# Kernel tuning notes

Hardware: AMD Instinct MI355X
Metric: run time of the kernel (lower is better)

The kernel has to match this reference:

```python
import jax, jax.numpy as jnp
import numpy as np

N = 200000          # number of nodes (objects)
H = 64              # hidden_size
ARITIES = [1, 2, 3] # arity per relation
NTUP = [250000, 250000, 250000]  # ground atoms per relation


def setup_inputs() -> dict:
    key = jax.random.key(0)
    ks = jax.random.split(key, 32)
    inp = {"node_states": jax.random.normal(ks[0], (N, H), jnp.float32)}
    i = 1
    for r, (a, t) in enumerate(zip(ARITIES, NTUP)):
        inp[f"rel{r}_idx"] = jax.random.randint(ks[i], (t * a,), 0, N, dtype=jnp.int32).astype(jnp.int64); i += 1
        d = a * H
        s = (2.0 / d) ** 0.5
        inp[f"w1_r{r}"] = jax.random.normal(ks[i], (d, d), jnp.float32) * s; i += 1
        inp[f"b1_r{r}"] = jnp.zeros((d,), jnp.float32)
        inp[f"w2_r{r}"] = jax.random.normal(ks[i], (d, d), jnp.float32) * s; i += 1
        inp[f"b2_r{r}"] = jnp.zeros((d,), jnp.float32)
    su = (1.0 / (2 * H)) ** 0.5
    inp["wu1"] = jax.random.normal(ks[i], (2 * H, 2 * H), jnp.float32) * su; i += 1
    inp["bu1"] = jnp.zeros((2 * H,), jnp.float32)
    inp["wu2"] = jax.random.normal(ks[i], (2 * H, H), jnp.float32) * su
    inp["bu2"] = jnp.zeros((H,), jnp.float32)
    return inp


def reference(node_states, rel0_idx, rel1_idx, rel2_idx,
              w1_r0, b1_r0, w2_r0, b2_r0,
              w1_r1, b1_r1, w2_r1, b2_r1,
              w1_r2, b1_r2, w2_r2, b2_r2,
              wu1, bu1, wu2, bu2):
    sum_msg = jnp.zeros_like(node_states)
    rels = [(ARITIES[0], rel0_idx, w1_r0, b1_r0, w2_r0, b2_r0),
            (ARITIES[1], rel1_idx, w1_r1, b1_r1, w2_r1, b2_r1),
            (ARITIES[2], rel2_idx, w1_r2, b1_r2, w2_r2, b2_r2)]
    for a, idx, w1, b1, w2, b2 in rels:
        # gather node states for each ground atom: [T, a*H]
        x = node_states[idx].reshape(-1, a * H)
        h = jax.nn.relu(x @ w1 + b1)
        msg = (h @ w2 + b2).reshape(-1, H)  # [T*a, H]
        # scatter-add messages back to their nodes
        sum_msg = sum_msg.at[idx].add(msg)
    z = jnp.concatenate([sum_msg, node_states], axis=1)  # [N, 2H]
    return jax.nn.relu(z @ wu1 + bu1) @ wu2 + bu2
```

## Files before the change

kernel.cpp:

```cpp
#include <hip/hip_runtime.h>

#define H 64

typedef __attribute__((ext_vector_type(8))) __bf16 bf16x8;
typedef __attribute__((ext_vector_type(4))) float f32x4;
typedef unsigned short u16;
typedef unsigned int u32;

union F8 { bf16x8 b; u16 u[8]; uint4 q; };

__device__ __forceinline__ u16 f2bf(float f) {
    union { __bf16 h; u16 u; } v; v.h = (__bf16)f; return v.u;
}
__device__ __forceinline__ float bf2f(u16 x) {
    return __uint_as_float((u32)x << 16);
}
__device__ __forceinline__ unsigned swz(int col, int k, int K) {
    return ((unsigned)(col * K + k) * 2u) ^ (((unsigned)col & 7u) << 4);
}

struct Seg { const float* src; unsigned dstBytes; int K; int N; };
struct Segs { Seg s[8]; };

__global__ __launch_bounds__(256) void conv_weights(Segs segs, char* out) {
    Seg sg = segs.s[blockIdx.y];
    int total = sg.K * sg.N;
    char* dst = out + sg.dstBytes;
    for (int e = blockIdx.x * 256 + threadIdx.x; e < total; e += gridDim.x * 256) {
        int k = e / sg.N, n = e % sg.N;
        *(u16*)(dst + swz(n, k, sg.K)) = f2bf(sg.src[e]);
    }
}

struct PrepA { const float4* nsrc; ushort4* ndst; int n4; Segs segs; char* wout; u32* cnt; int N; };

__global__ __launch_bounds__(256) void prep_kernel(PrepA a) {
    if (blockIdx.y == 0) {
        for (int i = blockIdx.x * 256 + threadIdx.x; i < a.n4; i += gridDim.x * 256) {
            float4 f = a.nsrc[i];
            ushort4 o;
            o.x = f2bf(f.x); o.y = f2bf(f.y); o.z = f2bf(f.z); o.w = f2bf(f.w);
            a.ndst[i] = o;
        }
    } else if (blockIdx.y == 1) {
        for (int s = 0; s < 8; ++s) {
            Seg sg = a.segs.s[s];
            int total = sg.K * sg.N;
            char* dst = a.wout + sg.dstBytes;
            for (int e = blockIdx.x * 256 + threadIdx.x; e < total; e += gridDim.x * 256) {
                int k = e / sg.N, n = e % sg.N;
                *(u16*)(dst + swz(n, k, sg.K)) = f2bf(sg.src[e]);
            }
        }
    } else {
        for (int i = blockIdx.x * 256 + threadIdx.x; i < a.N; i += gridDim.x * 256)
            a.cnt[i] = 0u;
    }
}

__global__ __launch_bounds__(512) void scan_blocks(u32* __restrict__ data,
                                                   u32* __restrict__ sums, int n) {
    __shared__ u32 s[512];
    int tid = threadIdx.x, i = blockIdx.x * 512 + tid;
    u32 v = (i < n) ? data[i] : 0u;
    s[tid] = v; __syncthreads();
    for (int d = 1; d < 512; d <<= 1) {
        u32 t = (tid >= d) ? s[tid - d] : 0u; __syncthreads();
        s[tid] += t; __syncthreads();
    }
    if (i < n) data[i] = s[tid] - v;
    if (tid == 511) sums[blockIdx.x] = s[511];
}

__global__ __launch_bounds__(512) void scan_sums(u32* __restrict__ sums, int nb) {
    __shared__ u32 s[512];
    int tid = threadIdx.x;
    u32 v = (tid < nb) ? sums[tid] : 0u;
    s[tid] = v; __syncthreads();
    for (int d = 1; d < 512; d <<= 1) {
        u32 t = (tid >= d) ? s[tid - d] : 0u; __syncthreads();
        s[tid] += t; __syncthreads();
    }
    if (tid < nb) sums[tid] = s[tid] - v;
}

__global__ __launch_bounds__(512) void scan_add(u32* __restrict__ data,
                                                const u32* __restrict__ sums, int n) {
    int i = blockIdx.x * 512 + threadIdx.x;
    if (i < n) data[i] += sums[blockIdx.x];
}

struct OFix {
    const int* idx0; const int* idx1; const int* idx2;
    int m0, m1, m2;
    const u32* base; const u32* pre; u32* ord;
};

__global__ __launch_bounds__(256) void ord_fix(OFix a) {
    const int Mtot = a.m0 + a.m1 + a.m2;
    for (int e = blockIdx.x * 256 + threadIdx.x; e < Mtot; e += gridDim.x * 256) {
        int lm = e, node;
        if (lm < a.m0) node = a.idx0[lm];
        else { lm -= a.m0; if (lm < a.m1) node = a.idx1[lm]; else node = a.idx2[lm - a.m1]; }
        a.ord[a.base[node] + a.pre[e]] = (u32)e;
    }
}

struct Scat {
    const int* idx0; const int* idx1; const int* idx2;
    int m0, m1, m2;
    const u32* base; const u32* pre;
    const u16* msgu; u16* msgs;
};

__global__ __launch_bounds__(256) void scatter_msg(Scat a) {
    const int Mtot = a.m0 + a.m1 + a.m2;
    const int CH = Mtot * 8;
    for (int c = blockIdx.x * 256 + threadIdx.x; c < CH; c += gridDim.x * 256) {
        const int e = c >> 3, q = c & 7;
        int lm = e, node;
        if (lm < a.m0) node = a.idx0[lm];
        else { lm -= a.m0; if (lm < a.m1) node = a.idx1[lm]; else node = a.idx2[lm - a.m1]; }
        const u32 slot = a.base[node] + a.pre[e];
        ((uint4*)(a.msgs + (size_t)slot * 64))[q] =
            ((const uint4*)(a.msgu + (size_t)e * 64))[q];
    }
}

template<int A>
__device__ __forceinline__ void msg_body(
    const u16* __restrict__ nsb, const int* __restrict__ idx,
    const u16* __restrict__ w1T, const float* __restrict__ b1,
    const u16* __restrict__ w2T, const float* __restrict__ b2,
    u16* __restrict__ msgR, int T, int bid, u16* Wl, u16* h1)
{
    constexpr int D    = A * 64;
    constexpr int KS   = D / 32;
    constexpr int NT   = D / 16;
    constexpr bool DUAL = (A == 1);
    constexpr bool CS   = (A > 1);
    constexpr int RF   = CS ? 2 : 1;
    constexpr int WH   = (A == 3) ? 3 : 1;
    constexpr int NTH  = NT / WH;
    constexpr int NTW  = CS ? NTH / 2 : NTH;
    constexpr int COLH = D / WH;
    constexpr int NPF  = (DUAL ? 2 * D * D : COLH * D) / 8 / 512;
    constexpr int NB   = WH * NTW;

    const int tid  = threadIdx.x;
    const int lane = tid & 63;
    const int w    = tid >> 6;
    const int g    = lane >> 4;
    const int lr   = lane & 15;
    const int rg   = CS ? (w >> 1) : w;
    const int cg   = CS ? (w & 1) : 0;

    const int tile = bid * 128;

    auto stage = [&](const u16* gsrc) {
#pragma unroll
        for (int i = 0; i < NPF; ++i) {
            const u16* gp = gsrc + ((i * 512 + tid) << 3);
            u16* lp = Wl + ((i * 512 + (w << 6)) << 3);
            __builtin_amdgcn_global_load_lds(
                (const __attribute__((address_space(1))) void*)gp,
                (__attribute__((address_space(3))) void*)lp, 16, 0, 0);
        }
    };

    bf16x8 a1[RF][KS];
#pragma unroll
    for (int rf = 0; rf < RF; ++rf) {
        const int trow = tile + rg * (16 * RF) + rf * 16 + lr;
        const int tl   = trow < T ? trow : T - 1;
        int nodes[A];
#pragma unroll
        for (int s = 0; s < A; ++s) nodes[s] = idx[(long)tl * A + s];
#pragma unroll
        for (int kk = 0; kk < KS; ++kk) {
            const u16* p = nsb + (long)nodes[kk >> 1] * H + ((kk & 1) * 32 + g * 8);
            F8 t; t.q = *(const uint4*)p;
            a1[rf][kk] = t.b;
        }
    }

    float bias1[NB], bias2[NB];
#pragma unroll
    for (int i = 0; i < NB; ++i) {
        const int jg = (i / NTW) * NTH + cg * NTW + (i % NTW);
        bias1[i] = b1[jg * 16 + lr];
        bias2[i] = b2[jg * 16 + lr];
    }

#pragma unroll
    for (int hh = 0; hh < WH; ++hh) {
        stage(DUAL ? w1T : (w1T + (size_t)hh * COLH * D));
        asm volatile("s_waitcnt vmcnt(0)" ::: "memory");
        __syncthreads();

#pragma unroll
        for (int jl = 0; jl < NTW; ++jl) {
            const int jc = cg * NTW + jl;
            const int jg = hh * NTH + jc;
            f32x4 acc0 = {0.f, 0.f, 0.f, 0.f};
            f32x4 acc1 = {0.f, 0.f, 0.f, 0.f};
#pragma unroll
            for (int kk = 0; kk < KS; ++kk) {
                F8 bf; bf.q = *(const uint4*)((const char*)Wl + swz(jc * 16 + lr, kk * 32 + g * 8, D));
                acc0 = __builtin_amdgcn_mfma_f32_16x16x32_bf16(a1[0][kk], bf.b, acc0, 0, 0, 0);
                if constexpr (CS)
                    acc1 = __builtin_amdgcn_mfma_f32_16x16x32_bf16(a1[1][kk], bf.b, acc1, 0, 0, 0);
            }
#pragma unroll
            for (int r = 0; r < 4; ++r) {
                const int row0 = rg * (16 * RF) + g * 4 + r;
                float v0 = acc0[r] + bias1[hh * NTW + jl]; v0 = v0 > 0.f ? v0 : 0.f;
                *(u16*)((char*)h1 + swz(row0, jg * 16 + lr, D)) = f2bf(v0);
                if constexpr (CS) {
                    float v1 = acc1[r] + bias1[hh * NTW + jl]; v1 = v1 > 0.f ? v1 : 0.f;
                    *(u16*)((char*)h1 + swz(row0 + 16, jg * 16 + lr, D)) = f2bf(v1);
                }
            }
        }
        if constexpr (!DUAL) __syncthreads();
    }

    bf16x8 a2[RF][KS];
#pragma unroll
    for (int rf = 0; rf < RF; ++rf) {
        const int row = rg * (16 * RF) + rf * 16 + lr;
#pragma unroll
        for (int kk = 0; kk < KS; ++kk) {
            F8 t; t.q = *(const uint4*)((const char*)h1 + swz(row, kk * 32 + g * 8, D));
            a2[rf][kk] = t.b;
        }
    }

#pragma unroll
    for (int hh = 0; hh < WH; ++hh) {
        if constexpr (!DUAL) {
            stage(w2T + (size_t)hh * COLH * D);
            asm volatile("s_waitcnt vmcnt(0)" ::: "memory");
            __syncthreads();
        }
        const char* W2base = DUAL ? (const char*)(Wl + D * D) : (const char*)Wl;

#pragma unroll
        for (int jl = 0; jl < NTW; ++jl) {
            const int jc = cg * NTW + jl;
            const int jg = hh * NTH + jc;
            f32x4 acc0 = {0.f, 0.f, 0.f, 0.f};
            f32x4 acc1 = {0.f, 0.f, 0.f, 0.f};
#pragma unroll
            for (int kk = 0; kk < KS; ++kk) {
                F8 bf; bf.q = *(const uint4*)(W2base + swz(jc * 16 + lr, kk * 32 + g * 8, D));
                acc0 = __builtin_amdgcn_mfma_f32_16x16x32_bf16(a2[0][kk], bf.b, acc0, 0, 0, 0);
                if constexpr (CS)
                    acc1 = __builtin_amdgcn_mfma_f32_16x16x32_bf16(a2[1][kk], bf.b, acc1, 0, 0, 0);
            }
            const int gc   = jg * 16 + lr;
            const int slot = gc >> 6;
            const int cs_  = gc & 63;
#pragma unroll
            for (int r = 0; r < 4; ++r) {
                const int a0 = rg * (16 * RF) + g * 4 + r;
                const int m0 = a0 * A + slot;
                unsigned b0 = (((unsigned)(m0 * 64 + cs_)) * 2u) ^ (((unsigned)m0 & 7u) << 4);
                *(u16*)((char*)h1 + b0) = f2bf(acc0[r] + bias2[hh * NTW + jl]);
                if constexpr (CS) {
                    const int m1 = (a0 + 16) * A + slot;
                    unsigned b1x = (((unsigned)(m1 * 64 + cs_)) * 2u) ^ (((unsigned)m1 & 7u) << 4);
                    *(u16*)((char*)h1 + b1x) = f2bf(acc1[r] + bias2[hh * NTW + jl]);
                }
            }
        }
        if constexpr (!DUAL) { if (hh + 1 < WH) __syncthreads(); }
    }

    if constexpr (CS) {
        __syncthreads();
        const int mbase = tile * A;
        constexpr int CH = 128 * A * 16;
#pragma unroll
        for (int i = 0; i < CH / 512; ++i) {
            const int c    = i * 512 + tid;
            const int row  = c >> 4;
            const int atom = row / A;
            if (tile + atom < T) {
                unsigned byte = (((unsigned)(row * 64 + (c & 15) * 4)) * 2u) ^ (((unsigned)row & 7u) << 4);
                uint2 v = *(const uint2*)((const char*)h1 + byte);
                *(uint2*)(msgR + (size_t)(mbase + row) * 64 + (c & 15) * 4) = v;
            }
        }
    } else {
        const bool full  = (tile + 128 <= T);
#pragma unroll
        for (int i = 0; i < 16 * A; i += 4) {
            int ml   = i + (lane >> 4);
            int mrow = w * 16 * A + ml;
            bool ok  = full || ((tile + w * 16 + ml / A) < T);
            if (ok) {
                unsigned byte = (((unsigned)(mrow * 64 + (lane & 15) * 4)) * 2u) ^ (((unsigned)mrow & 7u) << 4);
                uint2 v = *(const uint2*)((const char*)h1 + byte);
                *(uint2*)(msgR + (size_t)((tile * A) + mrow) * 64 + (lane & 15) * 4) = v;
            }
        }
    }
}

struct MegaA {
    const u16* nsb;
    const int* idx0; const int* idx1; const int* idx2;
    int m0, m1, m2, t0, t1, t2;
    u32* cnt; u32* pre;
    const u16 *w10, *w20, *w11, *w21, *w12, *w22;
    const float *b10, *b20, *b11, *b21, *b12, *b22;
    u16* msgu;
    int nrank, nb2, nb1, nb0, striped;
};

__global__ __launch_bounds__(512, 4) void mega_kernel(MegaA a) {
    __shared__ __align__(16) u16 sm[36864];
    const int bx = blockIdx.x;
    int kind, id;
    if (a.striped) {
        const int strip = 4 * a.nrank;
        if (bx < strip) {
            if ((bx & 3) == 3) { kind = 1; id = bx >> 2; }
            else               { kind = 0; id = bx - (bx >> 2); }
        } else { kind = 0; id = bx - a.nrank; }
    } else {
        if (bx < a.nrank) { kind = 1; id = bx; }
        else              { kind = 0; id = bx - a.nrank; }
    }

    if (kind == 1) {
        const int Mtot = a.m0 + a.m1 + a.m2;
        for (int e = id * 512 + (int)threadIdx.x; e < Mtot; e += a.nrank * 512) {
            int lm = e, node;
            if (lm < a.m0) node = a.idx0[lm];
            else { lm -= a.m0; if (lm < a.m1) node = a.idx1[lm]; else node = a.idx2[lm - a.m1]; }
            a.pre[e] = atomicAdd(a.cnt + node, 1u);
        }
        return;
    }

    const int nmsg = a.nb2 + a.nb1 + a.nb0;
    if (id >= nmsg) return;
    if (id < a.nb2)
        msg_body<3>(a.nsb, a.idx2, a.w12, a.b12, a.w22, a.b22,
                    a.msgu + (size_t)(a.m0 + a.m1) * 64, a.t2, id, sm, sm + 12288);
    else if (id < a.nb2 + a.nb1)
        msg_body<2>(a.nsb, a.idx1, a.w11, a.b11, a.w21, a.b21,
                    a.msgu + (size_t)a.m0 * 64, a.t1, id - a.nb2, sm, sm + 16384);
    else
        msg_body<1>(a.nsb, a.idx0, a.w10, a.b10, a.w20, a.b20,
                    a.msgu, a.t0, id - a.nb2 - a.nb1, sm, sm + 8192);
}

template<int A>
__global__ __launch_bounds__(512) void rel_kernel(
    const float* __restrict__ ns, const int* __restrict__ idx,
    const u16* __restrict__ w1T, const float* __restrict__ b1,
    const u16* __restrict__ w2T, const float* __restrict__ b2,
    float* __restrict__ dout, int T)
{
    constexpr int D  = A * 64;
    constexpr int KS = D / 32;
    constexpr int NT = D / 16;
    constexpr bool DUAL = (A == 1);
    __shared__ __align__(16) u16 Wl[(DUAL ? 2 : 1) * D * D];
    __shared__ __align__(16) u16 h1[128 * D];

    const int tid  = threadIdx.x;
    const int lane = tid & 63;
    const int w    = tid >> 6;
    const int g    = lane >> 4;
    const int lr   = lane & 15;

    const int tile = blockIdx.x * 128;
    const int trow = tile + w * 16 + lr;
    const int tl   = trow < T ? trow : T - 1;

    {
        constexpr int NV = (DUAL ? 2 : 1) * D * D / 8;
        const uint4* s4 = (const uint4*)w1T;
        uint4* d4 = (uint4*)Wl;
#pragma unroll
        for (int i = 0; i < NV / 512; ++i) d4[i * 512 + tid] = s4[i * 512 + tid];
    }

    int nodes[A];
#pragma unroll
    for (int s = 0; s < A; ++s) nodes[s] = idx[(long)tl * A + s];

    bf16x8 a1[KS];
#pragma unroll
    for (int kk = 0; kk < KS; ++kk) {
        const float* p = ns + (long)nodes[kk >> 1] * H + ((kk & 1) * 32 + g * 8);
        float4 f0 = *(const float4*)p;
        float4 f1 = *(const float4*)(p + 4);
        F8 t;
        t.u[0] = f2bf(f0.x); t.u[1] = f2bf(f0.y); t.u[2] = f2bf(f0.z); t.u[3] = f2bf(f0.w);
        t.u[4] = f2bf(f1.x); t.u[5] = f2bf(f1.y); t.u[6] = f2bf(f1.z); t.u[7] = f2bf(f1.w);
        a1[kk] = t.b;
    }

    float bias1[NT];
#pragma unroll
    for (int j = 0; j < NT; ++j) bias1[j] = b1[j * 16 + lr];

    __syncthreads();

#pragma unroll
    for (int j = 0; j < NT; ++j) {
        f32x4 acc = {0.f, 0.f, 0.f, 0.f};
#pragma unroll
        for (int kk = 0; kk < KS; ++kk) {
            F8 bf; bf.q = *(const uint4*)((const char*)Wl + swz(j * 16 + lr, kk * 32 + g * 8, D));
            acc = __builtin_amdgcn_mfma_f32_16x16x32_bf16(a1[kk], bf.b, acc, 0, 0, 0);
        }
#pragma unroll
        for (int r = 0; r < 4; ++r) {
            float vv = acc[r] + bias1[j];
            vv = vv > 0.f ? vv : 0.f;
            int row = w * 16 + g * 4 + r;
            *(u16*)((char*)h1 + swz(row, j * 16 + lr, D)) = f2bf(vv);
        }
    }

    const char* W2base;
    if constexpr (!DUAL) {
        __syncthreads();
        const uint4* s4 = (const uint4*)w2T;
        uint4* d4 = (uint4*)Wl;
        constexpr int NV = D * D / 8;
#pragma unroll
        for (int i = 0; i < NV / 512; ++i) d4[i * 512 + tid] = s4[i * 512 + tid];
        W2base = (const char*)Wl;
    } else {
        W2base = (const char*)(Wl + D * D);
    }

    bf16x8 a2[KS];
#pragma unroll
    for (int kk = 0; kk < KS; ++kk) {
        int row = w * 16 + lr;
        F8 t; t.q = *(const uint4*)((const char*)h1 + swz(row, kk * 32 + g * 8, D));
        a2[kk] = t.b;
    }

    float bias2[NT];
#pragma unroll
    for (int j = 0; j < NT; ++j) bias2[j] = b2[j * 16 + lr];

    int  nodes2[A][4];
    bool pred[4];
#pragma unroll
    for (int r = 0; r < 4; ++r) {
        int t  = tile + w * 16 + g * 4 + r;
        int tc = t < T ? t : T - 1;
        pred[r] = t < T;
#pragma unroll
        for (int s = 0; s < A; ++s) nodes2[s][r] = idx[(long)tc * A + s];
    }
    if constexpr (!DUAL) __syncthreads();

#pragma unroll
    for (int j = 0; j < NT; ++j) {
        f32x4 acc = {0.f, 0.f, 0.f, 0.f};
#pragma unroll
        for (int kk = 0; kk < KS; ++kk) {
            F8 bf; bf.q = *(const uint4*)(W2base + swz(j * 16 + lr, kk * 32 + g * 8, D));
            acc = __builtin_amdgcn_mfma_f32_16x16x32_bf16(a2[kk], bf.b, acc, 0, 0, 0);
        }
        const int slot = j >> 2;
        const int coff = (j & 3) * 16 + lr;
#pragma unroll
        for (int r = 0; r < 4; ++r) {
            if (pred[r])
                unsafeAtomicAdd(dout + (long)nodes2[slot][r] * H + coff, acc[r] + bias2[j]);
        }
    }
}

template<int MODE>
__global__ __launch_bounds__(512) void update_kernel(
    const float* __restrict__ ns, const u16* __restrict__ nsb,
    const float* __restrict__ sum,
    const u32* __restrict__ ord, const u32* __restrict__ base,
    const u16* __restrict__ msg, int Mtot,
    const u16* __restrict__ wu1T, const float* __restrict__ bu1,
    const u16* __restrict__ wu2T, const float* __restrict__ bu2,
    float* __restrict__ out, int N)
{
    __shared__ __align__(16) u16 Wl[128 * 128 + 64 * 128];
    __shared__ __align__(16) u16 h[128 * 128];

    const int tid  = threadIdx.x;
    const int lane = tid & 63;
    const int w    = tid >> 6;
    const int g    = lane >> 4;
    const int lr   = lane & 15;

    {
        const uint4* s4 = (const uint4*)wu1T;
        uint4* d4 = (uint4*)Wl;
#pragma unroll
        for (int i = 0; i < 6; ++i) d4[i * 512 + tid] = s4[i * 512 + tid];
    }

    const int tile = blockIdx.x * 128;
    const int trow = tile + w * 16 + lr;
    const int tl   = trow < N ? trow : N - 1;

    bf16x8 a1[4];
    if constexpr (MODE <= 1) {
        const u32 s = base[tl];
        const u32 e = (tl + 1 < N) ? base[tl + 1] : (u32)Mtot;
        float s0[8], s1[8];
#pragma unroll
        for (int j = 0; j < 8; ++j) { s0[j] = 0.f; s1[j] = 0.f; }
        for (u32 p = s; p < e; ++p) {
            const u16* row = msg + (size_t)(MODE == 1 ? ord[p] : p) * 64;
            F8 v0, v1;
            v0.q = *(const uint4*)(row + g * 8);
            v1.q = *(const uint4*)(row + 32 + g * 8);
#pragma unroll
            for (int j = 0; j < 8; ++j) { s0[j] += bf2f(v0.u[j]); s1[j] += bf2f(v1.u[j]); }
        }
        F8 t0, t1;
#pragma unroll
        for (int j = 0; j < 8; ++j) { t0.u[j] = f2bf(s0[j]); t1.u[j] = f2bf(s1[j]); }
        a1[0] = t0.b; a1[1] = t1.b;
    } else {
#pragma unroll
        for (int kk = 0; kk < 2; ++kk) {
            int k = kk * 32 + g * 8;
            const float* p = sum + (long)tl * H + k;
            float4 f0 = *(const float4*)p;
            float4 f1 = *(const float4*)(p + 4);
            F8 t;
            t.u[0] = f2bf(f0.x); t.u[1] = f2bf(f0.y); t.u[2] = f2bf(f0.z); t.u[3] = f2bf(f0.w);
            t.u[4] = f2bf(f1.x); t.u[5] = f2bf(f1.y); t.u[6] = f2bf(f1.z); t.u[7] = f2bf(f1.w);
            a1[kk] = t.b;
        }
    }
#pragma unroll
    for (int kk = 2; kk < 4; ++kk) {
        if constexpr (MODE <= 1) {
            const u16* prow = nsb + (long)tl * H;
            F8 t; t.q = *(const uint4*)(prow + (kk - 2) * 32 + g * 8);
            a1[kk] = t.b;
        } else {
            int k = (kk - 2) * 32 + g * 8;
            const float* p = ns + (long)tl * H + k;
            float4 f0 = *(const float4*)p;
            float4 f1 = *(const float4*)(p + 4);
            F8 t;
            t.u[0] = f2bf(f0.x); t.u[1] = f2bf(f0.y); t.u[2] = f2bf(f0.z); t.u[3] = f2bf(f0.w);
            t.u[4] = f2bf(f1.x); t.u[5] = f2bf(f1.y); t.u[6] = f2bf(f1.z); t.u[7] = f2bf(f1.w);
            a1[kk] = t.b;
        }
    }

    float bias1[8], bias2[4];
#pragma unroll
    for (int j = 0; j < 8; ++j) bias1[j] = bu1[j * 16 + lr];
#pragma unroll
    for (int j = 0; j < 4; ++j) bias2[j] = bu2[j * 16 + lr];

    __syncthreads();

#pragma unroll
    for (int j = 0; j < 8; ++j) {
        f32x4 acc = {0.f, 0.f, 0.f, 0.f};
#pragma unroll
        for (int kk = 0; kk < 4; ++kk) {
            F8 bf; bf.q = *(const uint4*)((const char*)Wl + swz(j * 16 + lr, kk * 32 + g * 8, 128));
            acc = __builtin_amdgcn_mfma_f32_16x16x32_bf16(a1[kk], bf.b, acc, 0, 0, 0);
        }
#pragma unroll
        for (int r = 0; r < 4; ++r) {
            float vv = acc[r] + bias1[j];
            vv = vv > 0.f ? vv : 0.f;
            int row = w * 16 + g * 4 + r;
            *(u16*)((char*)h + swz(row, j * 16 + lr, 128)) = f2bf(vv);
        }
    }

    bf16x8 a2[4];
#pragma unroll
    for (int kk = 0; kk < 4; ++kk) {
        int row = w * 16 + lr;
        F8 t; t.q = *(const uint4*)((const char*)h + swz(row, kk * 32 + g * 8, 128));
        a2[kk] = t.b;
    }

    const char* W2base = (const char*)(Wl + 128 * 128);
#pragma unroll
    for (int j = 0; j < 4; ++j) {
        f32x4 acc = {0.f, 0.f, 0.f, 0.f};
#pragma unroll
        for (int kk = 0; kk < 4; ++kk) {
            F8 bf; bf.q = *(const uint4*)(W2base + swz(j * 16 + lr, kk * 32 + g * 8, 128));
            acc = __builtin_amdgcn_mfma_f32_16x16x32_bf16(a2[kk], bf.b, acc, 0, 0, 0);
        }
#pragma unroll
        for (int r = 0; r < 4; ++r) {
            int t = tile + w * 16 + g * 4 + r;
            if (t < N) out[(long)t * H + j * 16 + lr] = acc[r] + bias2[j];
        }
    }
}

extern "C" void kernel_launch(void* const* d_in, const int* in_sizes, int n_in,
                              void* d_out, int out_size, void* d_ws, size_t ws_size,
                              hipStream_t stream) {
    const float* ns = (const float*)d_in[0];
    const int* idxs[3] = { (const int*)d_in[1], (const int*)d_in[6], (const int*)d_in[11] };
    const float* b1s[3] = { (const float*)d_in[3], (const float*)d_in[8], (const float*)d_in[13] };
    const float* b2s[3] = { (const float*)d_in[5], (const float*)d_in[10], (const float*)d_in[15] };
    const float* bu1 = (const float*)d_in[17];
    const float* bu2 = (const float*)d_in[19];

    const int N = in_sizes[0] / H;
    const int Ts[3] = { in_sizes[1], in_sizes[6] / 2, in_sizes[11] / 3 };
    const int Ms[3] = { Ts[0] * 1, Ts[1] * 2, Ts[2] * 3 };
    const long Mtot = (long)Ms[0] + Ms[1] + Ms[2];

    char* wsb = (char*)d_ws;
    auto AL = [](size_t x) { return (x + 255) & ~(size_t)255; };

    const unsigned O_W1R0 = 0;
    const unsigned O_W2R0 = O_W1R0 + 64 * 64 * 2;
    const unsigned O_W1R1 = O_W2R0 + 64 * 64 * 2;
    const unsigned O_W2R1 = O_W1R1 + 128 * 128 * 2;
    const unsigned O_W1R2 = O_W2R1 + 128 * 128 * 2;
    const unsigned O_W2R2 = O_W1R2 + 192 * 192 * 2;
    const unsigned O_WU1  = O_W2R2 + 192 * 192 * 2;
    const unsigned O_WU2  = O_WU1 + 128 * 128 * 2;
    const size_t  wEnd    = O_WU2 + 128 * 64 * 2;
    const unsigned wOff1[3] = { O_W1R0, O_W1R1, O_W1R2 };
    const unsigned wOff2[3] = { O_W2R0, O_W2R1, O_W2R2 };

    const int nb = (N + 511) / 512;

    const size_t O_CNT = AL(wEnd);
    const size_t O_SUM = AL(O_CNT + (size_t)N * 4);
    const size_t O_PRE = AL(O_SUM + (size_t)nb * 4);
    const size_t O_ORD = AL(O_PRE + (size_t)Mtot * 4);
    const size_t O_NSB = AL(O_ORD + (size_t)Mtot * 4);
    const size_t nsLen = (size_t)N * H * 2;
    const size_t O_MSG = AL(O_NSB + nsLen);
    const size_t O_MSGS = AL(O_MSG + (size_t)Mtot * 128);
    const size_t need1 = O_MSGS;
    const size_t need2 = O_MSGS + (size_t)Mtot * 128;

    const bool sorted2 = (nb <= 512) && (ws_size >= need2);
    const bool sorted1 = (nb <= 512) && (ws_size >= need1);

    Segs segs;
    segs.s[0] = {(const float*)d_in[2],  O_W1R0, 64, 64};
    segs.s[1] = {(const float*)d_in[4],  O_W2R0, 64, 64};
    segs.s[2] = {(const float*)d_in[7],  O_W1R1, 128, 128};
    segs.s[3] = {(const float*)d_in[9],  O_W2R1, 128, 128};
    segs.s[4] = {(const float*)d_in[12], O_W1R2, 192, 192};
    segs.s[5] = {(const float*)d_in[14], O_W2R2, 192, 192};
    segs.s[6] = {(const float*)d_in[16], O_WU1, 128, 128};
    segs.s[7] = {(const float*)d_in[18], O_WU2, 128, 64};

    float* dout = (float*)d_out;
    const u16* W1[3] = { (const u16*)(wsb + wOff1[0]), (const u16*)(wsb + wOff1[1]), (const u16*)(wsb + wOff1[2]) };
    const u16* W2[3] = { (const u16*)(wsb + wOff2[0]), (const u16*)(wsb + wOff2[1]), (const u16*)(wsb + wOff2[2]) };

    auto gT = [](int T) { return (T + 127) / 128; };

    if (sorted1 || sorted2) {
        u32* cnt = (u32*)(wsb + O_CNT);
        u32* sums = (u32*)(wsb + O_SUM);
        u32* pre = (u32*)(wsb + O_PRE);
        u32* ord = (u32*)(wsb + O_ORD);
        u16* nsbp = (u16*)(wsb + O_NSB);
        u16* msgu = (u16*)(wsb + O_MSG);
        u16* msgs = (u16*)(wsb + O_MSGS);

        PrepA pp;
        pp.nsrc = (const float4*)ns; pp.ndst = (ushort4*)nsbp; pp.n4 = N * H / 4;
        pp.segs = segs; pp.wout = wsb; pp.cnt = cnt; pp.N = N;
        prep_kernel<<<dim3(448, 3), 256, 0, stream>>>(pp);

        const int nb0 = gT(Ts[0]), nb1 = gT(Ts[1]), nb2 = gT(Ts[2]);
        const int nmsg = nb0 + nb1 + nb2;
        int NR = nmsg / 3; if (NR > 1024) NR = 1024; if (NR < 1) NR = 1;
        const int striped = (nmsg >= 3 * NR) ? 1 : 0;
        const int NTOT = NR + nmsg;

        MegaA ma;
        ma.nsb = nsbp;
        ma.idx0 = idxs[0]; ma.idx1 = idxs[1]; ma.idx2 = idxs[2];
        ma.m0 = Ms[0]; ma.m1 = Ms[1]; ma.m2 = Ms[2];
        ma.t0 = Ts[0]; ma.t1 = Ts[1]; ma.t2 = Ts[2];
        ma.cnt = cnt; ma.pre = pre;
        ma.w10 = W1[0]; ma.w20 = W2[0];
        ma.w11 = W1[1]; ma.w21 = W2[1];
        ma.w12 = W1[2]; ma.w22 = W2[2];
        ma.b10 = b1s[0]; ma.b20 = b2s[0];
        ma.b11 = b1s[1]; ma.b21 = b2s[1];
        ma.b12 = b1s[2]; ma.b22 = b2s[2];
        ma.msgu = msgu;
        ma.nrank = NR; ma.nb2 = nb2; ma.nb1 = nb1; ma.nb0 = nb0; ma.striped = striped;
        mega_kernel<<<NTOT, 512, 0, stream>>>(ma);

        scan_blocks<<<nb, 512, 0, stream>>>(cnt, sums, N);
        scan_sums<<<1, 512, 0, stream>>>(sums, nb);
        scan_add<<<nb, 512, 0, stream>>>(cnt, sums, N);

        if (sorted2) {
            Scat sc;
            sc.idx0 = idxs[0]; sc.idx1 = idxs[1]; sc.idx2 = idxs[2];
            sc.m0 = Ms[0]; sc.m1 = Ms[1]; sc.m2 = Ms[2];
            sc.base = cnt; sc.pre = pre;
            sc.msgu = msgu; sc.msgs = msgs;
            scatter_msg<<<2048, 256, 0, stream>>>(sc);

            update_kernel<0><<<(N + 127) / 128, 512, 0, stream>>>(
                ns, nsbp, nullptr, nullptr, cnt, msgs, (int)Mtot,
                (const u16*)(wsb + O_WU1), bu1, (const u16*)(wsb + O_WU2), bu2, dout, N);
        } else {
            OFix fx;
            fx.idx0 = idxs[0]; fx.idx1 = idxs[1]; fx.idx2 = idxs[2];
            fx.m0 = Ms[0]; fx.m1 = Ms[1]; fx.m2 = Ms[2];
            fx.base = cnt; fx.pre = pre; fx.ord = ord;
            ord_fix<<<2048, 256, 0, stream>>>(fx);

            update_kernel<1><<<(N + 127) / 128, 512, 0, stream>>>(
                ns, nsbp, nullptr, ord, cnt, msgu, (int)Mtot,
                (const u16*)(wsb + O_WU1), bu1, (const u16*)(wsb + O_WU2), bu2, dout, N);
        }
    } else {
        conv_weights<<<dim3(36, 8), 256, 0, stream>>>(segs, wsb);
        hipMemsetAsync(dout, 0, (size_t)N * H * sizeof(float), stream);
        for (int r = 0; r < 3; ++r) {
            const int T = Ts[r], nbl = gT(T);
            if (r == 0) rel_kernel<1><<<nbl, 512, 0, stream>>>(ns, idxs[0], W1[0], b1s[0], W2[0], b2s[0], dout, T);
            if (r == 1) rel_kernel<2><<<nbl, 512, 0, stream>>>(ns, idxs[1], W1[1], b1s[1], W2[1], b2s[1], dout, T);
            if (r == 2) rel_kernel<3><<<nbl, 512, 0, stream>>>(ns, idxs[2], W1[2], b1s[2], W2[2], b2s[2], dout, T);
        }
        update_kernel<2><<<(N + 127) / 128, 512, 0, stream>>>(
            ns, nullptr, dout, nullptr, nullptr, nullptr, 0,
            (const u16*)(wsb + O_WU1), bu1, (const u16*)(wsb + O_WU2), bu2, dout, N);
    }
}
```

Before: 268.9 us.

## Use 1024-thread blocks in mega kernel with doubled arity-1 tile

Raises the message/rank mega kernel from 512 to 1024 threads per block and reorganizes warps as row groups times column groups (4 column groups for arity 2/3, 2 for arity 1). Arity 1 now processes 256 atoms per block, so its weight staging is amortized over twice as many rows. All arities now use the two-row-fragment path and a unified LDS-to-global copy-out, with an extra barrier added for the dual-weight case. It risks higher register pressure under launch_bounds(1024,6), heavier barriers with 16 waves, and LDS limits on residency.

```diff
diff --git a/kernel.cpp b/kernel.cpp
--- a/kernel.cpp
+++ b/kernel.cpp
@@ -138,13 +138,13 @@
     constexpr int KS   = D / 32;
     constexpr int NT   = D / 16;
     constexpr bool DUAL = (A == 1);
-    constexpr bool CS   = (A > 1);
-    constexpr int RF   = CS ? 2 : 1;
+    constexpr int TILE = DUAL ? 256 : 128;
     constexpr int WH   = (A == 3) ? 3 : 1;
     constexpr int NTH  = NT / WH;
-    constexpr int NTW  = CS ? NTH / 2 : NTH;
+    constexpr int CG   = DUAL ? 2 : 4;
+    constexpr int NTW  = NTH / CG;
     constexpr int COLH = D / WH;
-    constexpr int NPF  = (DUAL ? 2 * D * D : COLH * D) / 8 / 512;
+    constexpr int NV4  = (DUAL ? 2 * D * D : COLH * D) / 8;
     constexpr int NB   = WH * NTW;
 
     const int tid  = threadIdx.x;
@@ -152,26 +152,29 @@
     const int w    = tid >> 6;
     const int g    = lane >> 4;
     const int lr   = lane & 15;
-    const int rg   = CS ? (w >> 1) : w;
-    const int cg   = CS ? (w & 1) : 0;
-
-    const int tile = bid * 128;
+    const int rg   = w / CG;
+    const int cg   = w % CG;
+
+    const int tile = bid * TILE;
 
     auto stage = [&](const u16* gsrc) {
 #pragma unroll
-        for (int i = 0; i < NPF; ++i) {
-            const u16* gp = gsrc + ((i * 512 + tid) << 3);
-            u16* lp = Wl + ((i * 512 + (w << 6)) << 3);
-            __builtin_amdgcn_global_load_lds(
-                (const __attribute__((address_space(1))) void*)gp,
-                (__attribute__((address_space(3))) void*)lp, 16, 0, 0);
+        for (int i = 0; i < (NV4 + 1023) / 1024; ++i) {
+            const int ob = i * 1024 + (w << 6);
+            if (ob < NV4) {
+                const u16* gp = gsrc + ((i * 1024 + tid) << 3);
+                u16* lp = Wl + ((size_t)ob << 3);
+                __builtin_amdgcn_global_load_lds(
+                    (const __attribute__((address_space(1))) void*)gp,
+                    (__attribute__((address_space(3))) void*)lp, 16, 0, 0);
+            }
         }
     };
 
-    bf16x8 a1[RF][KS];
-#pragma unroll
-    for (int rf = 0; rf < RF; ++rf) {
-        const int trow = tile + rg * (16 * RF) + rf * 16 + lr;
+    bf16x8 a1[2][KS];
+#pragma unroll
+    for (int rf = 0; rf < 2; ++rf) {
+        const int trow = tile + rg * 32 + rf * 16 + lr;
         const int tl   = trow < T ? trow : T - 1;
         int nodes[A];
 #pragma unroll
@@ -208,33 +211,31 @@
             for (int kk = 0; kk < KS; ++kk) {
                 F8 bf; bf.q = *(const uint4*)((const char*)Wl + swz(jc * 16 + lr, kk * 32 + g * 8, D));
                 acc0 = __builtin_amdgcn_mfma_f32_16x16x32_bf16(a1[0][kk], bf.b, acc0, 0, 0, 0);
-                if constexpr (CS)
-                    acc1 = __builtin_amdgcn_mfma_f32_16x16x32_bf16(a1[1][kk], bf.b, acc1, 0, 0, 0);
+                acc1 = __builtin_amdgcn_mfma_f32_16x16x32_bf16(a1[1][kk], bf.b, acc1, 0, 0, 0);
             }
 #pragma unroll
             for (int r = 0; r < 4; ++r) {
-                const int row0 = rg * (16 * RF) + g * 4 + r;
+                const int row0 = rg * 32 + g * 4 + r;
                 float v0 = acc0[r] + bias1[hh * NTW + jl]; v0 = v0 > 0.f ? v0 : 0.f;
-                *(u16*)((char*)h1 + swz(row0, jg * 16 + lr, D)) = f2bf(v0);
-                if constexpr (CS) {
-                    float v1 = acc1[r] + bias1[hh * NTW + jl]; v1 = v1 > 0.f ? v1 : 0.f;
-                    *(u16*)((char*)h1 + swz(row0 + 16, jg * 16 + lr, D)) = f2bf(v1);
-                }
+                float v1 = acc1[r] + bias1[hh * NTW + jl]; v1 = v1 > 0.f ? v1 : 0.f;
+                *(u16*)((char*)h1 + swz(row0,      jg * 16 + lr, D)) = f2bf(v0);
+                *(u16*)((char*)h1 + swz(row0 + 16, jg * 16 + lr, D)) = f2bf(v1);
             }
         }
-        if constexpr (!DUAL) __syncthreads();
-    }
-
-    bf16x8 a2[RF][KS];
-#pragma unroll
-    for (int rf = 0; rf < RF; ++rf) {
-        const int row = rg * (16 * RF) + rf * 16 + lr;
+        __syncthreads();
+    }
+
+    bf16x8 a2[2][KS];
+#pragma unroll
+    for (int rf = 0; rf < 2; ++rf) {
+        const int row = rg * 32 + rf * 16 + lr;
 #pragma unroll
         for (int kk = 0; kk < KS; ++kk) {
             F8 t; t.q = *(const uint4*)((const char*)h1 + swz(row, kk * 32 + g * 8, D));
             a2[rf][kk] = t.b;
         }
     }
+    if constexpr (DUAL) __syncthreads();
 
 #pragma unroll
     for (int hh = 0; hh < WH; ++hh) {
@@ -255,55 +256,37 @@
             for (int kk = 0; kk < KS; ++kk) {
                 F8 bf; bf.q = *(const uint4*)(W2base + swz(jc * 16 + lr, kk * 32 + g * 8, D));
                 acc0 = __builtin_amdgcn_mfma_f32_16x16x32_bf16(a2[0][kk], bf.b, acc0, 0, 0, 0);
-                if constexpr (CS)
-                    acc1 = __builtin_amdgcn_mfma_f32_16x16x32_bf16(a2[1][kk], bf.b, acc1, 0, 0, 0);
+                acc1 = __builtin_amdgcn_mfma_f32_16x16x32_bf16(a2[1][kk], bf.b, acc1, 0, 0, 0);
             }
             const int gc   = jg * 16 + lr;
             const int slot = gc >> 6;
             const int cs_  = gc & 63;
 #pragma unroll
             for (int r = 0; r < 4; ++r) {
-                const int a0 = rg * (16 * RF) + g * 4 + r;
+                const int a0 = rg * 32 + g * 4 + r;
                 const int m0 = a0 * A + slot;
+                const int m1 = (a0 + 16) * A + slot;
                 unsigned b0 = (((unsigned)(m0 * 64 + cs_)) * 2u) ^ (((unsigned)m0 & 7u) << 4);
+                unsigned b1x = (((unsigned)(m1 * 64 + cs_)) * 2u) ^ (((unsigned)m1 & 7u) << 4);
                 *(u16*)((char*)h1 + b0) = f2bf(acc0[r] + bias2[hh * NTW + jl]);
-                if constexpr (CS) {
-                    const int m1 = (a0 + 16) * A + slot;
-                    unsigned b1x = (((unsigned)(m1 * 64 + cs_)) * 2u) ^ (((unsigned)m1 & 7u) << 4);
-                    *(u16*)((char*)h1 + b1x) = f2bf(acc1[r] + bias2[hh * NTW + jl]);
-                }
+                *(u16*)((char*)h1 + b1x) = f2bf(acc1[r] + bias2[hh * NTW + jl]);
             }
         }
         if constexpr (!DUAL) { if (hh + 1 < WH) __syncthreads(); }
     }
 
-    if constexpr (CS) {
-        __syncthreads();
-        const int mbase = tile * A;
-        constexpr int CH = 128 * A * 16;
-#pragma unroll
-        for (int i = 0; i < CH / 512; ++i) {
-            const int c    = i * 512 + tid;
-            const int row  = c >> 4;
-            const int atom = row / A;
-            if (tile + atom < T) {
-                unsigned byte = (((unsigned)(row * 64 + (c & 15) * 4)) * 2u) ^ (((unsigned)row & 7u) << 4);
-                uint2 v = *(const uint2*)((const char*)h1 + byte);
-                *(uint2*)(msgR + (size_t)(mbase + row) * 64 + (c & 15) * 4) = v;
-            }
-        }
-    } else {
-        const bool full  = (tile + 128 <= T);
-#pragma unroll
-        for (int i = 0; i < 16 * A; i += 4) {
-            int ml   = i + (lane >> 4);
-            int mrow = w * 16 * A + ml;
-            bool ok  = full || ((tile + w * 16 + ml / A) < T);
-            if (ok) {
-                unsigned byte = (((unsigned)(mrow * 64 + (lane & 15) * 4)) * 2u) ^ (((unsigned)mrow & 7u) << 4);
-                uint2 v = *(const uint2*)((const char*)h1 + byte);
-                *(uint2*)(msgR + (size_t)((tile * A) + mrow) * 64 + (lane & 15) * 4) = v;
-            }
+    __syncthreads();
+    const int mbase = tile * A;
+    constexpr int CH = TILE * A * 16;
+#pragma unroll
+    for (int i = 0; i < CH / 1024; ++i) {
+        const int c    = i * 1024 + tid;
+        const int row  = c >> 4;
+        const int atom = row / A;
+        if (tile + atom < T) {
+            unsigned byte = (((unsigned)(row * 64 + (c & 15) * 4)) * 2u) ^ (((unsigned)row & 7u) << 4);
+            uint2 v = *(const uint2*)((const char*)h1 + byte);
+            *(uint2*)(msgR + (size_t)(mbase + row) * 64 + (c & 15) * 4) = v;
         }
     }
 }
@@ -319,7 +302,7 @@
     int nrank, nb2, nb1, nb0, striped;
 };
 
-__global__ __launch_bounds__(512, 4) void mega_kernel(MegaA a) {
+__global__ __launch_bounds__(1024, 6) void mega_kernel(MegaA a) {
     __shared__ __align__(16) u16 sm[36864];
     const int bx = blockIdx.x;
     int kind, id;
@@ -336,7 +319,7 @@
 
     if (kind == 1) {
         const int Mtot = a.m0 + a.m1 + a.m2;
-        for (int e = id * 512 + (int)threadIdx.x; e < Mtot; e += a.nrank * 512) {
+        for (int e = id * 1024 + (int)threadIdx.x; e < Mtot; e += a.nrank * 1024) {
             int lm = e, node;
             if (lm < a.m0) node = a.idx0[lm];
             else { lm -= a.m0; if (lm < a.m1) node = a.idx1[lm]; else node = a.idx2[lm - a.m1]; }
@@ -690,7 +673,8 @@
         pp.segs = segs; pp.wout = wsb; pp.cnt = cnt; pp.N = N;
         prep_kernel<<<dim3(448, 3), 256, 0, stream>>>(pp);
 
-        const int nb0 = gT(Ts[0]), nb1 = gT(Ts[1]), nb2 = gT(Ts[2]);
+        const int nb0 = (Ts[0] + 255) / 256;
+        const int nb1 = gT(Ts[1]), nb2 = gT(Ts[2]);
         const int nmsg = nb0 + nb1 + nb2;
         int NR = nmsg / 3; if (NR > 1024) NR = 1024; if (NR < 1) NR = 1;
         const int striped = (nmsg >= 3 * NR) ? 1 : 0;
@@ -710,7 +694,7 @@
         ma.b12 = b1s[2]; ma.b22 = b2s[2];
         ma.msgu = msgu;
         ma.nrank = NR; ma.nb2 = nb2; ma.nb1 = nb1; ma.nb0 = nb0; ma.striped = striped;
-        mega_kernel<<<NTOT, 512, 0, stream>>>(ma);
+        mega_kernel<<<NTOT, 1024, 0, stream>>>(ma);
 
         scan_blocks<<<nb, 512, 0, stream>>>(cnt, sums, N);
         scan_sums<<<1, 512, 0, stream>>>(sums, nb);
```

New measurement: 420.7 us. +56.5%, slower.
